# Performance work log

Hardware: AMD Instinct MI355X
Metric: run time of the kernel (lower is better)

Reference implementation:

```python
import jax, jax.numpy as jnp
import numpy as np

D_MODEL = 1024
N_HEADS = 16
HEAD_DIM = D_MODEL // N_HEADS


def setup_inputs() -> dict:
    key = jax.random.key(0)
    k1, k2, k3 = jax.random.split(key, 3)
    x = jax.random.normal(k1, (4, 2048, D_MODEL), dtype=jnp.float32)
    # per-head qkv Linear (bias=False): torch weight [3*head_dim, d_model];
    # store transposed and stacked over heads: [H, d_model, 3*head_dim]
    w_qkv = jax.random.normal(k2, (N_HEADS, D_MODEL, 3 * HEAD_DIM), dtype=jnp.float32) * (1.0 / np.sqrt(D_MODEL))
    # output Linear (bias=False), stored transposed: [d_model, d_model]
    w_out = jax.random.normal(k3, (D_MODEL, D_MODEL), dtype=jnp.float32) * (1.0 / np.sqrt(D_MODEL))
    return {"x": x, "w_qkv": w_qkv, "w_out": w_out}


def reference(x, w_qkv, w_out):
    hd = HEAD_DIM
    # all heads' qkv in one contraction: [B, H, S, 3*hd]
    qkv = jnp.einsum("bsd,hde->bhse", x, w_qkv)
    q, k, v = qkv[..., :hd], qkv[..., hd:2 * hd], qkv[..., 2 * hd:]
    scale = 1.0 / hd  # NOTE: original scales by 1/dk, not 1/sqrt(dk)
    scores = jnp.einsum("bhqe,bhke->bhqk", q, k) * scale
    attn = jax.nn.softmax(scores, axis=-1)
    z = jnp.einsum("bhqk,bhke->bhqe", attn, v)  # [B, H, S, hd]
    # concat heads along feature dim (head order = list order)
    b, h, s, _ = z.shape
    z = jnp.transpose(z, (0, 2, 1, 3)).reshape(b, s, h * hd)
    return z @ w_out
```

## Files before the change

### kernel.cpp

```cpp
#include <hip/hip_runtime.h>
#include <hip/hip_bf16.h>

typedef unsigned short u16;
typedef __attribute__((ext_vector_type(4))) float f32x4;
typedef __attribute__((ext_vector_type(16))) float f32x16;
typedef __attribute__((ext_vector_type(8))) short s16x8;
typedef __attribute__((ext_vector_type(4))) unsigned short u16x4;

static __device__ __forceinline__ u16 f32_to_bf16(float f) {
    union { float f; unsigned u; } v; v.f = f;
    unsigned r = v.u + 0x7FFF + ((v.u >> 16) & 1);
    return (u16)(r >> 16);
}

static __device__ __forceinline__ unsigned cvt_pk_bf16(float lo, float hi) {
    unsigned r;
    asm("v_cvt_pk_bf16_f32 %0, %1, %2" : "=v"(r) : "v"(lo), "v"(hi));
    return r;
}

static __device__ __forceinline__ void pswap2(unsigned &a, unsigned &b) {
#if defined(__has_builtin) && __has_builtin(__builtin_amdgcn_permlane32_swap)
    auto r = __builtin_amdgcn_permlane32_swap(a, b, false, false);
    a = r[0]; b = r[1];
#else
    asm volatile("v_permlane32_swap_b32 %0, %1" : "+v"(a), "+v"(b));
#endif
}

static __device__ __forceinline__ float xhalf_sum(float x) {
    unsigned a = __float_as_uint(x), b = a;
    pswap2(a, b);
    return __uint_as_float(a) + __uint_as_float(b);
}

static __device__ __forceinline__ float fexp2(float x) {
#if defined(__has_builtin) && __has_builtin(__builtin_amdgcn_exp2f)
    return __builtin_amdgcn_exp2f(x);
#else
    return exp2f(x);
#endif
}

#define GLOAD_LDS16(gptr, lptr) \
    __builtin_amdgcn_global_load_lds((const __attribute__((address_space(1))) void*)(gptr), \
                                     (__attribute__((address_space(3))) void*)(lptr), 16, 0, 0)


__global__ void cvt_f32_bf16(const float* __restrict__ in, u16* __restrict__ out, int n) {
    int i = (blockIdx.x * 256 + threadIdx.x) * 4;
    if (i + 3 < n) {
        f32x4 v = *(const f32x4*)(in + i);
        u16x4 o;
        o.x = f32_to_bf16(v.x); o.y = f32_to_bf16(v.y);
        o.z = f32_to_bf16(v.z); o.w = f32_to_bf16(v.w);
        *(u16x4*)(out + i) = o;
    }
}

__global__ void cvt_wqkvT(const float* __restrict__ w, u16* __restrict__ wt) {
    __shared__ float tile[32][33];
    const int b = blockIdx.x;
    const int kb = b & 31, eb = (b >> 5) % 6, h = b / 192;
    const int x = threadIdx.x & 31, y = threadIdx.x >> 5;
#pragma unroll
    for (int j = 0; j < 4; ++j) {
        int kl = y + j * 8;
        tile[kl][x] = w[((size_t)(h * 1024 + kb * 32 + kl)) * 192 + eb * 32 + x];
    }
    __syncthreads();
#pragma unroll
    for (int j = 0; j < 4; ++j) {
        int el = y + j * 8;
        wt[((size_t)(h * 192 + eb * 32 + el)) * 1024 + kb * 32 + x] = f32_to_bf16(tile[x][el]);
    }
}

__global__ void cvt_woutT(const float* __restrict__ w, u16* __restrict__ wt) {
    __shared__ float tile[32][33];
    const int b = blockIdx.x;
    const int kb = b & 31, nb = b >> 5;
    const int x = threadIdx.x & 31, y = threadIdx.x >> 5;
#pragma unroll
    for (int j = 0; j < 4; ++j) {
        int kl = y + j * 8;
        tile[kl][x] = w[((size_t)(kb * 32 + kl)) * 1024 + nb * 32 + x];
    }
    __syncthreads();
#pragma unroll
    for (int j = 0; j < 4; ++j) {
        int nl = y + j * 8;
        wt[((size_t)(nb * 32 + nl)) * 1024 + kb * 32 + x] = f32_to_bf16(tile[x][nl]);
    }
}


#define SWZ4(r) (((r) & 3) ^ (((r) >> 2) & 3))

template <int EPI>
__global__ __launch_bounds__(256, 3)
void gemm_bt(const u16* __restrict__ A, const u16* __restrict__ B,
             float* __restrict__ Cf, u16* __restrict__ Qb, u16* __restrict__ Kb,
             u16* __restrict__ Vt, int M, int N, int K) {
    __shared__ __align__(16) u16 lA[3 * 128 * 32];
    __shared__ __align__(16) u16 lB[3 * 128 * 32];

    const int t = threadIdx.x;
    const int lane = t & 63;
    const int wave = t >> 6;
    const int wr = wave >> 1, wc = wave & 1;
    const int l15 = lane & 15, g = lane >> 4;

    const int nwg = gridDim.x;
    const int cpx = nwg >> 3;
    const int orig = blockIdx.x;
    const int logical = (orig & 7) * cpx + (orig >> 3);

    const int nbx = N >> 7;
    const int bx = logical % nbx, by = logical / nbx;
    const int bm = by << 7, bn = bx << 7;

    f32x4 acc[4][4] = {};

    const int sr0 = t >> 2;
    const int ss  = t & 3;

    const u16* Abase = A + (size_t)bm * K;
    const u16* Bbase = B + (size_t)bn * K;

#define GSTAGE(bb, kt) do { \
    _Pragma("unroll") \
    for (int c = 0; c < 2; ++c) { \
        int r = sr0 + 64 * c; \
        int cl = ss ^ SWZ4(r); \
        GLOAD_LDS16(Abase + (size_t)r * K + (kt) + cl * 8, &lA[(bb) + (r * 4 + ss) * 8]); \
        GLOAD_LDS16(Bbase + (size_t)r * K + (kt) + cl * 8, &lB[(bb) + (r * 4 + ss) * 8]); \
    } } while (0)

    const int NT = K >> 5;

    GSTAGE(0, 0);
    GSTAGE(4096, 32);
    asm volatile("s_waitcnt vmcnt(4)" ::: "memory");
    __builtin_amdgcn_s_barrier();
    __builtin_amdgcn_sched_barrier(0);

    int i0 = 0, i1 = 4096, i2 = 8192;

    for (int ti = 0; ti < NT; ++ti) {
        if (ti + 2 < NT) GSTAGE(i2, (ti + 2) << 5);

        const u16* Ac = &lA[i0];
        const u16* Bc = &lB[i0];
        s16x8 a[4], b[4];
#pragma unroll
        for (int i = 0; i < 4; ++i) {
            int r = wr * 64 + i * 16 + l15;
            int sl = g ^ SWZ4(r);
            a[i] = *(const s16x8*)&Ac[(r * 4 + sl) * 8];
        }
#pragma unroll
        for (int j = 0; j < 4; ++j) {
            int r = wc * 64 + j * 16 + l15;
            int sl = g ^ SWZ4(r);
            b[j] = *(const s16x8*)&Bc[(r * 4 + sl) * 8];
        }
#pragma unroll
        for (int i = 0; i < 4; ++i)
#pragma unroll
            for (int j = 0; j < 4; ++j)
                acc[i][j] = __builtin_amdgcn_mfma_f32_16x16x32_bf16(b[j], a[i], acc[i][j], 0, 0, 0);

        if (ti + 1 < NT) {
            if (ti + 2 < NT) {
                asm volatile("s_waitcnt vmcnt(4)" ::: "memory");
            } else {
                asm volatile("s_waitcnt vmcnt(0)" ::: "memory");
            }
            __builtin_amdgcn_s_barrier();
            __builtin_amdgcn_sched_barrier(0);
        }
        int tmp = i0; i0 = i1; i1 = i2; i2 = tmp;
    }
#undef GSTAGE

    if constexpr (EPI == 0) {
#pragma unroll
        for (int i = 0; i < 4; ++i) {
            int m = bm + wr * 64 + i * 16 + l15;
#pragma unroll
            for (int j = 0; j < 4; ++j) {
                int n0 = bn + wc * 64 + j * 16 + g * 4;
                *(f32x4*)&Cf[(size_t)m * N + n0] = acc[i][j];
            }
        }
    } else {
        const float qscale = 0.022542110013890054f;
#pragma unroll
        for (int j = 0; j < 4; ++j) {
            int n0 = bn + wc * 64 + j * 16 + g * 4;
            int h = n0 / 192;
            int e0 = n0 - h * 192;
#pragma unroll
            for (int i = 0; i < 4; ++i) {
                int m = bm + wr * 64 + i * 16 + l15;
                int bb = m >> 11, s = m & 2047;
                int bh = bb * 16 + h;
                if (e0 < 64) {
                    u16x4 q;
#pragma unroll
                    for (int r = 0; r < 4; ++r) q[r] = f32_to_bf16(acc[i][j][r] * qscale);
                    *(u16x4*)&Qb[((size_t)bh * 2048 + s) * 64 + e0] = q;
                } else if (e0 < 128) {
                    u16x4 kk;
#pragma unroll
                    for (int r = 0; r < 4; ++r) kk[r] = f32_to_bf16(acc[i][j][r]);
                    *(u16x4*)&Kb[((size_t)bh * 2048 + s) * 64 + (e0 - 64)] = kk;
                } else {
#pragma unroll
                    for (int r = 0; r < 4; ++r)
                        Vt[((size_t)bh * 64 + (e0 - 128 + r)) * 2048 + s] = f32_to_bf16(acc[i][j][r]);
                }
            }
        }
    }
}

__global__ __launch_bounds__(512, 4)
void attn32(const u16* __restrict__ Qb, const u16* __restrict__ Kb,
            const u16* __restrict__ Vt, u16* __restrict__ Zb) {
    __shared__ __align__(16) u16 lK[3 * 64 * 64];
    __shared__ __align__(16) u16 lV[3 * 64 * 64];
    __shared__ float lds_l[8][32];

    const int t = threadIdx.x;
    const int lane = t & 63;
    const int w = t >> 6;
    const int l31 = lane & 31, hi = lane >> 5;
    const int r7 = l31 & 7;

    const int orig = blockIdx.x;
    const int logical = (orig & 7) * 64 + (orig >> 3);
    const int bh = logical >> 3;
    const int qt = logical & 7;
    const int q0 = qt * 256 + w * 32;

    const u16* Kbh = Kb + (size_t)bh * 2048 * 64;
    const u16* Vbh = Vt + (size_t)bh * 64 * 2048;

    const int lr = lane >> 3;
    const int lc = (lane & 7) ^ lr;

    const u16* Qp = Qb + ((size_t)bh * 2048 + q0 + l31) * 64 + hi * 8;
    s16x8 qf[4];
#pragma unroll
    for (int kd = 0; kd < 4; ++kd) qf[kd] = *(const s16x8*)(Qp + kd * 16);

    f32x16 o0 = {}, o1 = {};
    float l = 0.f;

#define STAGE(bb, kvn) do { \
    int gr = w * 8 + lr; \
    GLOAD_LDS16(Kbh + (size_t)((kvn) + gr) * 64 + lc * 8, \
                &lK[(bb) + w * 512 + lane * 8]); \
    GLOAD_LDS16(Vbh + (size_t)gr * 2048 + (kvn) + lc * 8, \
                &lV[(bb) + w * 512 + lane * 8]); \
    } while (0)

    STAGE(0, 0);
    STAGE(4096, 64);
    asm volatile("s_waitcnt vmcnt(2)" ::: "memory");
    __builtin_amdgcn_s_barrier();
    __builtin_amdgcn_sched_barrier(0);

    int i0 = 0, i1 = 4096, i2 = 8192;

    for (int ti = 0; ti < 32; ++ti) {
        if (ti + 2 < 32) STAGE(i2, (ti + 2) << 6);

        const u16* Kc = &lK[i0];
        const u16* Vc = &lV[i0];

        f32x16 p0 = {}, p1 = {};
        __builtin_amdgcn_s_setprio(1);
#pragma unroll
        for (int kd = 0; kd < 4; ++kd) {
            int cs = ((2 * kd + hi) ^ r7) * 8;
            s16x8 kf0 = *(const s16x8*)&Kc[l31 * 64 + cs];
            p0 = __builtin_amdgcn_mfma_f32_32x32x16_bf16(kf0, qf[kd], p0, 0, 0, 0);
            s16x8 kf1 = *(const s16x8*)&Kc[(l31 + 32) * 64 + cs];
            p1 = __builtin_amdgcn_mfma_f32_32x32x16_bf16(kf1, qf[kd], p1, 0, 0, 0);
        }
        __builtin_amdgcn_s_setprio(0);

        float rs0 = 0.f, rs1 = 0.f, rs2 = 0.f, rs3 = 0.f;
#pragma unroll
        for (int r = 0; r < 16; r += 4) {
            p0[r]     = fexp2(p0[r]);     rs0 += p0[r];
            p0[r + 1] = fexp2(p0[r + 1]); rs1 += p0[r + 1];
            p0[r + 2] = fexp2(p0[r + 2]); rs2 += p0[r + 2];
            p0[r + 3] = fexp2(p0[r + 3]); rs3 += p0[r + 3];
            p1[r]     = fexp2(p1[r]);     rs0 += p1[r];
            p1[r + 1] = fexp2(p1[r + 1]); rs1 += p1[r + 1];
            p1[r + 2] = fexp2(p1[r + 2]); rs2 += p1[r + 2];
            p1[r + 3] = fexp2(p1[r + 3]); rs3 += p1[r + 3];
        }
        l += xhalf_sum((rs0 + rs1) + (rs2 + rs3));

        union { unsigned u[8]; s16x8 v[2]; } pa0, pa1;
        {
            unsigned c0 = cvt_pk_bf16(p0[0],  p0[1]);
            unsigned c1 = cvt_pk_bf16(p0[2],  p0[3]);
            unsigned c2 = cvt_pk_bf16(p0[4],  p0[5]);
            unsigned c3 = cvt_pk_bf16(p0[6],  p0[7]);
            unsigned c4 = cvt_pk_bf16(p0[8],  p0[9]);
            unsigned c5 = cvt_pk_bf16(p0[10], p0[11]);
            unsigned c6 = cvt_pk_bf16(p0[12], p0[13]);
            unsigned c7 = cvt_pk_bf16(p0[14], p0[15]);
            pswap2(c0, c2); pswap2(c1, c3);
            pswap2(c4, c6); pswap2(c5, c7);
            pa0.u[0] = c0; pa0.u[1] = c1; pa0.u[2] = c2; pa0.u[3] = c3;
            pa0.u[4] = c4; pa0.u[5] = c5; pa0.u[6] = c6; pa0.u[7] = c7;
        }
        {
            unsigned c0 = cvt_pk_bf16(p1[0],  p1[1]);
            unsigned c1 = cvt_pk_bf16(p1[2],  p1[3]);
            unsigned c2 = cvt_pk_bf16(p1[4],  p1[5]);
            unsigned c3 = cvt_pk_bf16(p1[6],  p1[7]);
            unsigned c4 = cvt_pk_bf16(p1[8],  p1[9]);
            unsigned c5 = cvt_pk_bf16(p1[10], p1[11]);
            unsigned c6 = cvt_pk_bf16(p1[12], p1[13]);
            unsigned c7 = cvt_pk_bf16(p1[14], p1[15]);
            pswap2(c0, c2); pswap2(c1, c3);
            pswap2(c4, c6); pswap2(c5, c7);
            pa1.u[0] = c0; pa1.u[1] = c1; pa1.u[2] = c2; pa1.u[3] = c3;
            pa1.u[4] = c4; pa1.u[5] = c5; pa1.u[6] = c6; pa1.u[7] = c7;
        }

        __builtin_amdgcn_s_setprio(1);
#pragma unroll
        for (int ks = 0; ks < 4; ++ks) {
            s16x8 pav = (ks < 2) ? pa0.v[ks] : pa1.v[ks - 2];
            int cs = ((ks * 2 + hi) ^ r7) * 8;
            s16x8 vf0 = *(const s16x8*)&Vc[l31 * 64 + cs];
            o0 = __builtin_amdgcn_mfma_f32_32x32x16_bf16(pav, vf0, o0, 0, 0, 0);
            s16x8 vf1 = *(const s16x8*)&Vc[(l31 + 32) * 64 + cs];
            o1 = __builtin_amdgcn_mfma_f32_32x32x16_bf16(pav, vf1, o1, 0, 0, 0);
        }
        __builtin_amdgcn_s_setprio(0);

        if (ti + 1 < 32) {
            if (ti + 2 < 32) {
                asm volatile("s_waitcnt vmcnt(2)" ::: "memory");
            } else {
                asm volatile("s_waitcnt vmcnt(0)" ::: "memory");
            }
            __builtin_amdgcn_s_barrier();
            __builtin_amdgcn_sched_barrier(0);
        }
        int tmp = i0; i0 = i1; i1 = i2; i2 = tmp;
    }
#undef STAGE

    if (lane < 32) lds_l[w][l31] = l;
    __syncthreads();

    const int b = bh >> 4, h = bh & 15;
#pragma unroll
    for (int r = 0; r < 16; ++r) {
        int qrow = (r & 3) + 8 * (r >> 2) + 4 * hi;
        float inv = 1.0f / lds_l[w][qrow];
        size_t rowbase = ((size_t)(b * 2048 + q0 + qrow)) * 1024 + h * 64 + l31;
        Zb[rowbase]      = f32_to_bf16(o0[r] * inv);
        Zb[rowbase + 32] = f32_to_bf16(o1[r] * inv);
    }
}


extern "C" void kernel_launch(void* const* d_in, const int* in_sizes, int n_in,
                              void* d_out, int out_size, void* d_ws, size_t ws_size,
                              hipStream_t stream) {
    const float* x     = (const float*)d_in[0];
    const float* w_qkv = (const float*)d_in[1];
    const float* w_out = (const float*)d_in[2];
    float* out = (float*)d_out;

    char* ws = (char*)d_ws;
    u16* xb  = (u16*)ws; ws += (size_t)8192 * 1024 * 2;
    u16* wqT = (u16*)ws; ws += (size_t)3072 * 1024 * 2;
    u16* woT = (u16*)ws; ws += (size_t)1024 * 1024 * 2;
    u16* Qb  = (u16*)ws; ws += (size_t)64 * 2048 * 64 * 2;
    u16* Kb  = (u16*)ws; ws += (size_t)64 * 2048 * 64 * 2;
    u16* Vt  = (u16*)ws; ws += (size_t)64 * 2048 * 64 * 2;
    u16* Zb  = (u16*)ws; ws += (size_t)8192 * 1024 * 2;

    cvt_f32_bf16<<<dim3(8192), dim3(256), 0, stream>>>(x, xb, 8192 * 1024);
    cvt_wqkvT<<<dim3(3072), dim3(256), 0, stream>>>(w_qkv, wqT);
    cvt_woutT<<<dim3(1024), dim3(256), 0, stream>>>(w_out, woT);

    gemm_bt<1><<<dim3(64 * 24), dim3(256), 0, stream>>>(xb, wqT, nullptr, Qb, Kb, Vt,
                                                        8192, 3072, 1024);
    attn32<<<dim3(512), dim3(512), 0, stream>>>(Qb, Kb, Vt, Zb);
    gemm_bt<0><<<dim3(64 * 8), dim3(256), 0, stream>>>(Zb, woT, out, nullptr, nullptr, nullptr,
                                                       8192, 1024, 1024);
}
```

Baseline: 193.6 us.

## Software-pipeline PV MFMA of previous tile behind current QK and softmax

Restructures the attention inner loop so the P·V MFMAs for the previous KV tile are issued right after the current tile's QK^T MFMAs, before the exp/convert step. This lets matrix work overlap the transcendental and pack/permute VALU work. The K/V prefetch now goes after the barrier into the buffer just consumed, and each iteration waits on vmcnt(0) instead of vmcnt(2). That shortens how far ahead loads are issued and may expose more memory latency. An epilogue handles the last tile's P·V.

New measurement: 192.1 us. Within noise of the previous version (-0.7%).

```diff
diff --git a/kernel.cpp b/kernel.cpp
--- a/kernel.cpp
+++ b/kernel.cpp
@@ -258,6 +258,7 @@
 
     f32x16 o0 = {}, o1 = {};
     float l = 0.f;
+    s16x8 pv0, pv1, pv2, pv3;
 
 #define STAGE(bb, kvn) do { \
     int gr = w * 8 + lr; \
@@ -273,13 +274,10 @@
     __builtin_amdgcn_s_barrier();
     __builtin_amdgcn_sched_barrier(0);
 
-    int i0 = 0, i1 = 4096, i2 = 8192;
+    int i_cur = 0, i_nxt = 4096, i_prv = 8192;
 
     for (int ti = 0; ti < 32; ++ti) {
-        if (ti + 2 < 32) STAGE(i2, (ti + 2) << 6);
-
-        const u16* Kc = &lK[i0];
-        const u16* Vc = &lV[i0];
+        const u16* Kc = &lK[i_cur];
 
         f32x16 p0 = {}, p1 = {};
         __builtin_amdgcn_s_setprio(1);
@@ -292,6 +290,21 @@
             p1 = __builtin_amdgcn_mfma_f32_32x32x16_bf16(kf1, qf[kd], p1, 0, 0, 0);
         }
         __builtin_amdgcn_s_setprio(0);
+
+        if (ti > 0) {
+            const u16* Vc = &lV[i_prv];
+            __builtin_amdgcn_s_setprio(1);
+#pragma unroll
+            for (int ks = 0; ks < 4; ++ks) {
+                s16x8 pav = (ks == 0) ? pv0 : (ks == 1) ? pv1 : (ks == 2) ? pv2 : pv3;
+                int cs = ((ks * 2 + hi) ^ r7) * 8;
+                s16x8 vf0 = *(const s16x8*)&Vc[l31 * 64 + cs];
+                o0 = __builtin_amdgcn_mfma_f32_32x32x16_bf16(pav, vf0, o0, 0, 0, 0);
+                s16x8 vf1 = *(const s16x8*)&Vc[(l31 + 32) * 64 + cs];
+                o1 = __builtin_amdgcn_mfma_f32_32x32x16_bf16(pav, vf1, o1, 0, 0, 0);
+            }
+            __builtin_amdgcn_s_setprio(0);
+        }
 
         float rs0 = 0.f, rs1 = 0.f, rs2 = 0.f, rs3 = 0.f;
 #pragma unroll
@@ -307,7 +320,6 @@
         }
         l += xhalf_sum((rs0 + rs1) + (rs2 + rs3));
 
-        union { unsigned u[8]; s16x8 v[2]; } pa0, pa1;
         {
             unsigned c0 = cvt_pk_bf16(p0[0],  p0[1]);
             unsigned c1 = cvt_pk_bf16(p0[2],  p0[3]);
@@ -319,8 +331,10 @@
             unsigned c7 = cvt_pk_bf16(p0[14], p0[15]);
             pswap2(c0, c2); pswap2(c1, c3);
             pswap2(c4, c6); pswap2(c5, c7);
-            pa0.u[0] = c0; pa0.u[1] = c1; pa0.u[2] = c2; pa0.u[3] = c3;
-            pa0.u[4] = c4; pa0.u[5] = c5; pa0.u[6] = c6; pa0.u[7] = c7;
+            union { unsigned u[8]; s16x8 v[2]; } pa;
+            pa.u[0] = c0; pa.u[1] = c1; pa.u[2] = c2; pa.u[3] = c3;
+            pa.u[4] = c4; pa.u[5] = c5; pa.u[6] = c6; pa.u[7] = c7;
+            pv0 = pa.v[0]; pv1 = pa.v[1];
         }
         {
             unsigned c0 = cvt_pk_bf16(p1[0],  p1[1]);
@@ -333,32 +347,32 @@
             unsigned c7 = cvt_pk_bf16(p1[14], p1[15]);
             pswap2(c0, c2); pswap2(c1, c3);
             pswap2(c4, c6); pswap2(c5, c7);
-            pa1.u[0] = c0; pa1.u[1] = c1; pa1.u[2] = c2; pa1.u[3] = c3;
-            pa1.u[4] = c4; pa1.u[5] = c5; pa1.u[6] = c6; pa1.u[7] = c7;
-        }
-
-        __builtin_amdgcn_s_setprio(1);
+            union { unsigned u[8]; s16x8 v[2]; } pa;
+            pa.u[0] = c0; pa.u[1] = c1; pa.u[2] = c2; pa.u[3] = c3;
+            pa.u[4] = c4; pa.u[5] = c5; pa.u[6] = c6; pa.u[7] = c7;
+            pv2 = pa.v[0]; pv3 = pa.v[1];
+        }
+
+        if (ti + 1 < 32) {
+            asm volatile("s_waitcnt vmcnt(0)" ::: "memory");
+            __builtin_amdgcn_s_barrier();
+            __builtin_amdgcn_sched_barrier(0);
+            if (ti + 2 < 32) STAGE(i_prv, (ti + 2) << 6);
+        }
+        int tmp = i_prv; i_prv = i_cur; i_cur = i_nxt; i_nxt = tmp;
+    }
+
+    {
+        const u16* Vc = &lV[i_prv];
 #pragma unroll
         for (int ks = 0; ks < 4; ++ks) {
-            s16x8 pav = (ks < 2) ? pa0.v[ks] : pa1.v[ks - 2];
+            s16x8 pav = (ks == 0) ? pv0 : (ks == 1) ? pv1 : (ks == 2) ? pv2 : pv3;
             int cs = ((ks * 2 + hi) ^ r7) * 8;
             s16x8 vf0 = *(const s16x8*)&Vc[l31 * 64 + cs];
             o0 = __builtin_amdgcn_mfma_f32_32x32x16_bf16(pav, vf0, o0, 0, 0, 0);
             s16x8 vf1 = *(const s16x8*)&Vc[(l31 + 32) * 64 + cs];
             o1 = __builtin_amdgcn_mfma_f32_32x32x16_bf16(pav, vf1, o1, 0, 0, 0);
         }
-        __builtin_amdgcn_s_setprio(0);
-
-        if (ti + 1 < 32) {
-            if (ti + 2 < 32) {
-                asm volatile("s_waitcnt vmcnt(2)" ::: "memory");
-            } else {
-                asm volatile("s_waitcnt vmcnt(0)" ::: "memory");
-            }
-            __builtin_amdgcn_s_barrier();
-            __builtin_amdgcn_sched_barrier(0);
-        }
-        int tmp = i0; i0 = i1; i1 = i2; i2 = tmp;
     }
 #undef STAGE
 
```
